# Performance work log

Measured on AMD Instinct MI355X. Metric: run time of the kernel, lower is better.

## Reference

```python
import jax, jax.numpy as jnp
import numpy as np

TOP_K = 2  # matches init kwarg top_k


def setup_inputs() -> dict:
    key = jax.random.key(0)
    k1, k2, k3, k4 = jax.random.split(key, 4)
    B, S, D, E = 4, 2048, 1024, 8
    x = jax.random.normal(k1, (B, S, D), dtype=jnp.float32)
    w_gate = jax.random.normal(k2, (D, E), dtype=jnp.float32) * 0.02
    w1 = jax.random.normal(k3, (E, D, 4 * D), dtype=jnp.float32) * 0.02
    w2 = jax.random.normal(k4, (E, 4 * D, D), dtype=jnp.float32) * 0.02
    return {"x": x, "w_gate": w_gate, "w1": w1, "w2": w2}


def reference(x, w_gate, w1, w2):
    # x: [B, S, D]; w_gate: [D, E]; w1: [E, D, 4D]; w2: [E, 4D, D]
    B, S, D = x.shape
    E = w1.shape[0]
    xt = x.reshape(-1, D)                      # [T, D], T = B*S
    T = xt.shape[0]

    logits = xt @ w_gate                       # [T, E]
    topk_vals, topk_idx = jax.lax.top_k(logits, TOP_K)  # [T, K]
    gates = jax.nn.softmax(topk_vals, axis=-1)          # [T, K]

    # Combine weights per (token, expert): scatter the top-k gates.
    comb = jnp.zeros((T, E), dtype=x.dtype)
    comb = comb.at[jnp.arange(T)[:, None], topk_idx].add(gates)  # [T, E]

    # Dense per-expert FFN over all tokens, masked by combine weight.
    # (Loop over the small fixed expert count; each iteration is a big GEMM.)
    out = jnp.zeros_like(xt)
    for e in range(E):
        h = jax.nn.relu(xt @ w1[e])            # [T, 4D]
        y = h @ w2[e]                          # [T, D]
        out = out + comb[:, e:e + 1] * y
    return out.reshape(B, S, D)
```

## Files before the change

kernel.cpp:

```cpp
#include <hip/hip_runtime.h>
#include <hip/hip_bf16.h>


#define T_TOK   8192
#define DIM     1024
#define NEXP    8
#define HID     4096
#define NASSIGN (T_TOK * 2)

typedef unsigned short ushort_t;
typedef __attribute__((ext_vector_type(8))) short bfrag;
typedef __attribute__((ext_vector_type(4))) float f32x4;

__device__ __forceinline__ ushort_t f2bf(float f) {
    union { float f; unsigned int u; } v; v.f = f;
    unsigned int r = v.u + 0x7FFFu + ((v.u >> 16) & 1u);
    return (ushort_t)(r >> 16);
}

__device__ __forceinline__ void async_load16(const void* g, void* l) {
    __builtin_amdgcn_global_load_lds(
        (const __attribute__((address_space(1))) unsigned int*)g,
        (__attribute__((address_space(3))) unsigned int*)l, 16, 0, 0);
}

__global__ __launch_bounds__(256)
void route_kern(const float* __restrict__ x, const float* __restrict__ wg,
                ushort_t* __restrict__ x_bf, int* __restrict__ topk,
                float* __restrict__ gates, int* __restrict__ counts)
{
    const int w = threadIdx.x >> 6, lane = threadIdx.x & 63;
    const int t = blockIdx.x * 4 + w;
    const float* xr = x + (size_t)t * DIM;
    float acc[8];
#pragma unroll
    for (int e = 0; e < 8; ++e) acc[e] = 0.f;

#pragma unroll
    for (int it = 0; it < 4; ++it) {
        const int j = it * 256 + lane * 4;
        float4 xv = *(const float4*)(xr + j);
        ushort4 xb;
        xb.x = f2bf(xv.x); xb.y = f2bf(xv.y); xb.z = f2bf(xv.z); xb.w = f2bf(xv.w);
        *(ushort4*)(x_bf + (size_t)t * DIM + j) = xb;
        const float xs[4] = {xv.x, xv.y, xv.z, xv.w};
#pragma unroll
        for (int jj = 0; jj < 4; ++jj) {
            float4 g0 = *(const float4*)(wg + (size_t)(j + jj) * 8);
            float4 g1 = *(const float4*)(wg + (size_t)(j + jj) * 8 + 4);
            acc[0] += xs[jj] * g0.x; acc[1] += xs[jj] * g0.y;
            acc[2] += xs[jj] * g0.z; acc[3] += xs[jj] * g0.w;
            acc[4] += xs[jj] * g1.x; acc[5] += xs[jj] * g1.y;
            acc[6] += xs[jj] * g1.z; acc[7] += xs[jj] * g1.w;
        }
    }
#pragma unroll
    for (int d = 1; d < 64; d <<= 1)
#pragma unroll
        for (int e = 0; e < 8; ++e) acc[e] += __shfl_xor(acc[e], d);

    if (lane == 0) {
        int i0 = 0; float v0 = acc[0];
#pragma unroll
        for (int e = 1; e < 8; ++e) if (acc[e] > v0) { v0 = acc[e]; i0 = e; }
        int i1 = -1; float v1 = -1e30f;
#pragma unroll
        for (int e = 0; e < 8; ++e) if (e != i0 && acc[e] > v1) { v1 = acc[e]; i1 = e; }
        float ex = __expf(v1 - v0);
        float inv = 1.f / (1.f + ex);
        topk[t * 2] = i0; topk[t * 2 + 1] = i1;
        gates[t * 2] = inv; gates[t * 2 + 1] = ex * inv;
        atomicAdd(&counts[i0], 1);
        atomicAdd(&counts[i1], 1);
    }
}

__global__ void scan_kern(const int* __restrict__ counts, int* __restrict__ offs,
                          int* __restrict__ cursors)
{
    if (threadIdx.x == 0) {
        int o = 0;
        for (int e = 0; e < NEXP; ++e) { offs[e] = o; cursors[e] = o; o += counts[e]; }
        offs[NEXP] = o;
    }
}

__global__ __launch_bounds__(256)
void scatter_kern(const int* __restrict__ topk, const float* __restrict__ gates,
                  int* __restrict__ cursors, int* __restrict__ tok_c,
                  float* __restrict__ gate_c)
{
    const int t = blockIdx.x * 256 + threadIdx.x;
#pragma unroll
    for (int k = 0; k < 2; ++k) {
        int e = topk[t * 2 + k];
        int pos = atomicAdd(&cursors[e], 1);
        tok_c[pos] = t;
        gate_c[pos] = gates[t * 2 + k];
    }
}

__global__ __launch_bounds__(256)
void transp_kern(const float* __restrict__ in, ushort_t* __restrict__ out, int K, int N)
{
    __shared__ float tile[64][65];
    const int e = blockIdx.z;
    const size_t ibase = (size_t)e * K * N, obase = (size_t)e * N * K;
    const int k0 = blockIdx.y * 64, n0 = blockIdx.x * 64;
    const int tid = threadIdx.x;

    const int r = tid >> 4, c4 = (tid & 15) * 4;
#pragma unroll
    for (int p = 0; p < 4; ++p) {
        int kk = p * 16 + r;
        float4 v = *(const float4*)(in + ibase + (size_t)(k0 + kk) * N + n0 + c4);
        tile[kk][c4] = v.x; tile[kk][c4 + 1] = v.y; tile[kk][c4 + 2] = v.z; tile[kk][c4 + 3] = v.w;
    }
    __syncthreads();
    const int nr = tid >> 6, kc = tid & 63;
#pragma unroll
    for (int p = 0; p < 16; ++p) {
        int nn = p * 4 + nr;
        out[obase + (size_t)(n0 + nn) * K + k0 + kc] = f2bf(tile[kc][nn]);
    }
}

template <int STAGE>
__global__ __launch_bounds__(256)
void gemm_kern(const ushort_t* __restrict__ A, const ushort_t* __restrict__ Bt,
               ushort_t* __restrict__ Hout, float* __restrict__ Out,
               const int* __restrict__ eoff, const int* __restrict__ tok_c,
               const float* __restrict__ gate_c, int K, int N)
{
    __shared__ ushort_t ldsA[128 * 64];
    __shared__ ushort_t ldsB[128 * 64];

    const int e = blockIdx.z;
    const int base = eoff[e];
    const int cnt = eoff[e + 1] - base;
    const int m0 = blockIdx.y * 128;
    if (m0 >= cnt) return;
    const int n0 = blockIdx.x * 128;

    const int tid = threadIdx.x;
    const int w = tid >> 6, lane = tid & 63;
    const int lhi = lane >> 4, llo = lane & 15;

    const ushort_t* asrc[4];
    const ushort_t* bsrc[4];
    int ldsoff[4];
    const ushort_t* Bbase = Bt + (size_t)e * (size_t)N * (size_t)K;
#pragma unroll
    for (int i = 0; i < 4; ++i) {
        int ci = ((i * 4 + w) << 6) + lane;
        int r = ci >> 3;
        int cb = (ci & 7) << 4;
        int sb = cb ^ ((r & 7) << 4);
        int gr = m0 + r; if (gr >= cnt) gr = cnt - 1;
        size_t arow = (STAGE == 1) ? (size_t)tok_c[base + gr] * DIM
                                   : (size_t)(base + gr) * HID;
        asrc[i] = A + arow + (sb >> 1);
        bsrc[i] = Bbase + (size_t)(n0 + r) * K + (sb >> 1);
        ldsoff[i] = (i * 4 + w) << 10;
    }

    f32x4 acc[4][4];
#pragma unroll
    for (int m = 0; m < 4; ++m)
#pragma unroll
        for (int n = 0; n < 4; ++n) acc[m][n] = (f32x4)(0.f);

    const int wr = (w >> 1) << 6;
    const int wc = (w & 1) << 6;

    for (int k0 = 0; k0 < K; k0 += 64) {
#pragma unroll
        for (int i = 0; i < 4; ++i) {
            async_load16(asrc[i] + k0, (char*)ldsA + ldsoff[i]);
            async_load16(bsrc[i] + k0, (char*)ldsB + ldsoff[i]);
        }
        __syncthreads();
#pragma unroll
        for (int s = 0; s < 2; ++s) {
            bfrag a[4], b[4];
            const int kb = (s << 6) + (lhi << 4);
#pragma unroll
            for (int m = 0; m < 4; ++m) {
                int row = wr + (m << 4) + llo;
                a[m] = *(const bfrag*)((const char*)ldsA + row * 128 + (kb ^ ((row & 7) << 4)));
            }
#pragma unroll
            for (int n = 0; n < 4; ++n) {
                int row = wc + (n << 4) + llo;
                b[n] = *(const bfrag*)((const char*)ldsB + row * 128 + (kb ^ ((row & 7) << 4)));
            }
#pragma unroll
            for (int m = 0; m < 4; ++m)
#pragma unroll
                for (int n = 0; n < 4; ++n)
                    acc[m][n] = __builtin_amdgcn_mfma_f32_16x16x32_bf16(a[m], b[n], acc[m][n], 0, 0, 0);
        }
        __syncthreads();
    }

    if (STAGE == 1) {
#pragma unroll
        for (int m = 0; m < 4; ++m)
#pragma unroll
            for (int i = 0; i < 4; ++i) {
                int row = wr + (m << 4) + (lhi << 2) + i;
                int gr = m0 + row;
                if (gr >= cnt) continue;
                size_t rb = (size_t)(base + gr) * HID + n0 + wc;
#pragma unroll
                for (int n = 0; n < 4; ++n) {
                    float v = acc[m][n][i];
                    Hout[rb + (n << 4) + llo] = f2bf(v > 0.f ? v : 0.f);
                }
            }
    } else {
#pragma unroll
        for (int m = 0; m < 4; ++m)
#pragma unroll
            for (int i = 0; i < 4; ++i) {
                int row = wr + (m << 4) + (lhi << 2) + i;
                int gr = m0 + row;
                if (gr >= cnt) continue;
                int tok = tok_c[base + gr];
                float g = gate_c[base + gr];
                size_t rb = (size_t)tok * DIM + n0 + wc;
#pragma unroll
                for (int n = 0; n < 4; ++n)
                    atomicAdd(&Out[rb + (n << 4) + llo], g * acc[m][n][i]);
            }
    }
}

extern "C" void kernel_launch(void* const* d_in, const int* in_sizes, int n_in,
                              void* d_out, int out_size, void* d_ws, size_t ws_size,
                              hipStream_t stream)
{
    const float* x  = (const float*)d_in[0];
    const float* wg = (const float*)d_in[1];
    const float* w1 = (const float*)d_in[2];
    const float* w2 = (const float*)d_in[3];
    float* out = (float*)d_out;

    char* ws = (char*)d_ws;
    ushort_t* x_bf = (ushort_t*)(ws + 0);
    ushort_t* w1t  = (ushort_t*)(ws + 16777216);
    ushort_t* w2t  = (ushort_t*)(ws + 83886080);
    ushort_t* h    = (ushort_t*)(ws + 150994944);
    char* ctrl     = ws + 285212672;
    int*   topk    = (int*)(ctrl);
    float* gates   = (float*)(ctrl + 65536);
    int*   tok_c   = (int*)(ctrl + 131072);
    float* gate_c  = (float*)(ctrl + 196608);
    int*   counts  = (int*)(ctrl + 262144);
    int*   offs    = (int*)(ctrl + 262144 + 64);
    int*   cursors = (int*)(ctrl + 262144 + 128);

    hipMemsetAsync(counts, 0, NEXP * sizeof(int), stream);
    hipMemsetAsync(out, 0, (size_t)T_TOK * DIM * sizeof(float), stream);

    route_kern<<<T_TOK / 4, 256, 0, stream>>>(x, wg, x_bf, topk, gates, counts);
    transp_kern<<<dim3(HID / 64, DIM / 64, NEXP), 256, 0, stream>>>(w1, w1t, DIM, HID);
    transp_kern<<<dim3(DIM / 64, HID / 64, NEXP), 256, 0, stream>>>(w2, w2t, HID, DIM);
    scan_kern<<<1, 64, 0, stream>>>(counts, offs, cursors);
    scatter_kern<<<T_TOK / 256, 256, 0, stream>>>(topk, gates, cursors, tok_c, gate_c);

    gemm_kern<1><<<dim3(HID / 128, 64, NEXP), 256, 0, stream>>>(
        x_bf, w1t, h, nullptr, offs, tok_c, gate_c, DIM, HID);
    gemm_kern<2><<<dim3(DIM / 128, 64, NEXP), 256, 0, stream>>>(
        h, w2t, nullptr, out, offs, tok_c, gate_c, HID, DIM);
}
```

Before: 761.5 us.

## Use 256x256 double-buffered GEMM tiles with XCD-aware block remapping

```diff
diff --git a/kernel.cpp b/kernel.cpp
--- a/kernel.cpp
+++ b/kernel.cpp
@@ -6,7 +6,6 @@
 #define DIM     1024
 #define NEXP    8
 #define HID     4096
-#define NASSIGN (T_TOK * 2)
 
 typedef unsigned short ushort_t;
 typedef __attribute__((ext_vector_type(8))) short bfrag;
@@ -125,93 +124,113 @@
     }
 }
 
-template <int STAGE>
-__global__ __launch_bounds__(256)
-void gemm_kern(const ushort_t* __restrict__ A, const ushort_t* __restrict__ Bt,
-               ushort_t* __restrict__ Hout, float* __restrict__ Out,
-               const int* __restrict__ eoff, const int* __restrict__ tok_c,
-               const float* __restrict__ gate_c, int K, int N)
-{
-    __shared__ ushort_t ldsA[128 * 64];
-    __shared__ ushort_t ldsB[128 * 64];
-
-    const int e = blockIdx.z;
+template <int STAGE, int NT, int NBLK>
+__global__ __launch_bounds__(512, 1)
+void gemm256(const ushort_t* __restrict__ A, const ushort_t* __restrict__ Bt,
+             ushort_t* __restrict__ Hout, float* __restrict__ Out,
+             const int* __restrict__ eoff, const int* __restrict__ tok_c,
+             const float* __restrict__ gate_c)
+{
+    constexpr int K = NT * 64;
+    constexpr int N = NBLK * 256;
+    constexpr int MB = 32;
+    __shared__ ushort_t lds[2][2][256 * 64];
+
+    const int nb = NEXP * MB * NBLK;
+    const int orig = blockIdx.x;
+    const int lg = (orig & 7) * (nb >> 3) + (orig >> 3);
+    const int e = lg / (MB * NBLK);
+    const int rem = lg - e * (MB * NBLK);
+    const int mblk = rem / NBLK;
+    const int nblk = rem - mblk * NBLK;
+
     const int base = eoff[e];
     const int cnt = eoff[e + 1] - base;
-    const int m0 = blockIdx.y * 128;
+    const int m0 = mblk * 256;
     if (m0 >= cnt) return;
-    const int n0 = blockIdx.x * 128;
+    const int n0 = nblk * 256;
 
     const int tid = threadIdx.x;
     const int w = tid >> 6, lane = tid & 63;
     const int lhi = lane >> 4, llo = lane & 15;
-
+    const int wm = (w >> 2) << 7;
+    const int wn = (w & 3) << 6;
+
+    const ushort_t* Bbase = Bt + (size_t)e * (size_t)N * (size_t)K;
     const ushort_t* asrc[4];
     const ushort_t* bsrc[4];
-    int ldsoff[4];
-    const ushort_t* Bbase = Bt + (size_t)e * (size_t)N * (size_t)K;
+    int lbase[4];
 #pragma unroll
     for (int i = 0; i < 4; ++i) {
-        int ci = ((i * 4 + w) << 6) + lane;
+        int ci = i * 512 + tid;
         int r = ci >> 3;
-        int cb = (ci & 7) << 4;
-        int sb = cb ^ ((r & 7) << 4);
+        int sb = ((ci & 7) << 4) ^ ((r & 7) << 4);
         int gr = m0 + r; if (gr >= cnt) gr = cnt - 1;
-        size_t arow = (STAGE == 1) ? (size_t)tok_c[base + gr] * DIM
-                                   : (size_t)(base + gr) * HID;
+        size_t arow = (STAGE == 1) ? (size_t)tok_c[base + gr] * (size_t)K
+                                   : (size_t)(base + gr) * (size_t)K;
         asrc[i] = A + arow + (sb >> 1);
         bsrc[i] = Bbase + (size_t)(n0 + r) * K + (sb >> 1);
-        ldsoff[i] = (i * 4 + w) << 10;
-    }
-
-    f32x4 acc[4][4];
-#pragma unroll
-    for (int m = 0; m < 4; ++m)
+        lbase[i] = (i * 8 + w) << 10;
+    }
+
+    f32x4 acc[8][4];
+#pragma unroll
+    for (int m = 0; m < 8; ++m)
 #pragma unroll
         for (int n = 0; n < 4; ++n) acc[m][n] = (f32x4)(0.f);
 
-    const int wr = (w >> 1) << 6;
-    const int wc = (w & 1) << 6;
-
-    for (int k0 = 0; k0 < K; k0 += 64) {
-#pragma unroll
-        for (int i = 0; i < 4; ++i) {
-            async_load16(asrc[i] + k0, (char*)ldsA + ldsoff[i]);
-            async_load16(bsrc[i] + k0, (char*)ldsB + ldsoff[i]);
+#pragma unroll
+    for (int i = 0; i < 4; ++i) {
+        async_load16(asrc[i], (char*)lds[0][0] + lbase[i]);
+        async_load16(bsrc[i], (char*)lds[0][1] + lbase[i]);
+    }
+    __syncthreads();
+
+    int cur = 0;
+    for (int t = 0; t < NT; ++t) {
+        if (t + 1 < NT) {
+            const int k0 = (t + 1) << 6;
+#pragma unroll
+            for (int i = 0; i < 4; ++i) {
+                async_load16(asrc[i] + k0, (char*)lds[cur ^ 1][0] + lbase[i]);
+                async_load16(bsrc[i] + k0, (char*)lds[cur ^ 1][1] + lbase[i]);
+            }
         }
-        __syncthreads();
-#pragma unroll
-        for (int s = 0; s < 2; ++s) {
-            bfrag a[4], b[4];
-            const int kb = (s << 6) + (lhi << 4);
-#pragma unroll
-            for (int m = 0; m < 4; ++m) {
-                int row = wr + (m << 4) + llo;
-                a[m] = *(const bfrag*)((const char*)ldsA + row * 128 + (kb ^ ((row & 7) << 4)));
+        const char* pA = (const char*)lds[cur][0];
+        const char* pB = (const char*)lds[cur][1];
+#pragma unroll
+        for (int ks = 0; ks < 2; ++ks) {
+            const int kb = (ks << 6) + (lhi << 4);
+            bfrag a[8], b[4];
+#pragma unroll
+            for (int m = 0; m < 8; ++m) {
+                int row = wm + (m << 4) + llo;
+                a[m] = *(const bfrag*)(pA + row * 128 + (kb ^ ((row & 7) << 4)));
             }
 #pragma unroll
             for (int n = 0; n < 4; ++n) {
-                int row = wc + (n << 4) + llo;
-                b[n] = *(const bfrag*)((const char*)ldsB + row * 128 + (kb ^ ((row & 7) << 4)));
-            }
-#pragma unroll
-            for (int m = 0; m < 4; ++m)
+                int row = wn + (n << 4) + llo;
+                b[n] = *(const bfrag*)(pB + row * 128 + (kb ^ ((row & 7) << 4)));
+            }
+#pragma unroll
+            for (int m = 0; m < 8; ++m)
 #pragma unroll
                 for (int n = 0; n < 4; ++n)
                     acc[m][n] = __builtin_amdgcn_mfma_f32_16x16x32_bf16(a[m], b[n], acc[m][n], 0, 0, 0);
         }
         __syncthreads();
+        cur ^= 1;
     }
 
     if (STAGE == 1) {
 #pragma unroll
-        for (int m = 0; m < 4; ++m)
+        for (int m = 0; m < 8; ++m)
 #pragma unroll
             for (int i = 0; i < 4; ++i) {
-                int row = wr + (m << 4) + (lhi << 2) + i;
+                int row = wm + (m << 4) + (lhi << 2) + i;
                 int gr = m0 + row;
                 if (gr >= cnt) continue;
-                size_t rb = (size_t)(base + gr) * HID + n0 + wc;
+                size_t rb = (size_t)(base + gr) * (size_t)N + n0 + wn;
 #pragma unroll
                 for (int n = 0; n < 4; ++n) {
                     float v = acc[m][n][i];
@@ -220,15 +239,15 @@
             }
     } else {
 #pragma unroll
-        for (int m = 0; m < 4; ++m)
+        for (int m = 0; m < 8; ++m)
 #pragma unroll
             for (int i = 0; i < 4; ++i) {
-                int row = wr + (m << 4) + (lhi << 2) + i;
+                int row = wm + (m << 4) + (lhi << 2) + i;
                 int gr = m0 + row;
                 if (gr >= cnt) continue;
                 int tok = tok_c[base + gr];
                 float g = gate_c[base + gr];
-                size_t rb = (size_t)tok * DIM + n0 + wc;
+                size_t rb = (size_t)tok * (size_t)N + n0 + wn;
 #pragma unroll
                 for (int n = 0; n < 4; ++n)
                     atomicAdd(&Out[rb + (n << 4) + llo], g * acc[m][n][i]);
@@ -269,8 +288,8 @@
     scan_kern<<<1, 64, 0, stream>>>(counts, offs, cursors);
     scatter_kern<<<T_TOK / 256, 256, 0, stream>>>(topk, gates, cursors, tok_c, gate_c);
 
-    gemm_kern<1><<<dim3(HID / 128, 64, NEXP), 256, 0, stream>>>(
-        x_bf, w1t, h, nullptr, offs, tok_c, gate_c, DIM, HID);
-    gemm_kern<2><<<dim3(DIM / 128, 64, NEXP), 256, 0, stream>>>(
-        h, w2t, nullptr, out, offs, tok_c, gate_c, HID, DIM);
-}
+    gemm256<1, 16, 16><<<NEXP * 32 * 16, 512, 0, stream>>>(
+        x_bf, w1t, h, nullptr, offs, tok_c, gate_c);
+    gemm256<2, 64, 4><<<NEXP * 32 * 4, 512, 0, stream>>>(
+        h, w2t, nullptr, out, offs, tok_c, gate_c);
+}
```

After: 765.3 us. Within noise of the previous version (+0.5%).

## Add split-K for down-projection, XCD-aware block remap, and vectorized transpose stores

Applied to the files above, without the earlier changes.

```diff
diff --git a/kernel.cpp b/kernel.cpp
--- a/kernel.cpp
+++ b/kernel.cpp
@@ -6,7 +6,6 @@
 #define DIM     1024
 #define NEXP    8
 #define HID     4096
-#define NASSIGN (T_TOK * 2)
 
 typedef unsigned short ushort_t;
 typedef __attribute__((ext_vector_type(8))) short bfrag;
@@ -117,30 +116,44 @@
         tile[kk][c4] = v.x; tile[kk][c4 + 1] = v.y; tile[kk][c4 + 2] = v.z; tile[kk][c4 + 3] = v.w;
     }
     __syncthreads();
-    const int nr = tid >> 6, kc = tid & 63;
-#pragma unroll
-    for (int p = 0; p < 16; ++p) {
-        int nn = p * 4 + nr;
-        out[obase + (size_t)(n0 + nn) * K + k0 + kc] = f2bf(tile[kc][nn]);
-    }
-}
-
-template <int STAGE>
+    const int k8 = (tid & 7) * 8, nr = tid >> 3;
+#pragma unroll
+    for (int p = 0; p < 2; ++p) {
+        int nn = p * 32 + nr;
+        bfrag v;
+#pragma unroll
+        for (int j = 0; j < 8; ++j) v[j] = (short)f2bf(tile[k8 + j][nn]);
+        *(bfrag*)(out + obase + (size_t)(n0 + nn) * K + k0 + k8) = v;
+    }
+}
+
+template <int STAGE, int NTK, int NBF, int SPLITK, int KF, int NF>
 __global__ __launch_bounds__(256)
 void gemm_kern(const ushort_t* __restrict__ A, const ushort_t* __restrict__ Bt,
                ushort_t* __restrict__ Hout, float* __restrict__ Out,
                const int* __restrict__ eoff, const int* __restrict__ tok_c,
-               const float* __restrict__ gate_c, int K, int N)
-{
+               const float* __restrict__ gate_c)
+{
+    constexpr int MBF = 64;
     __shared__ ushort_t ldsA[128 * 64];
     __shared__ ushort_t ldsB[128 * 64];
 
-    const int e = blockIdx.z;
+    constexpr int nb = NEXP * MBF * NBF;
+    const int orig = blockIdx.x;
+    const int lg = (orig & 7) * (nb >> 3) + (orig >> 3);
+    const int e = lg / (MBF * NBF);
+    const int rem = lg - e * (MBF * NBF);
+    const int mblk = rem / NBF;
+    const int nidx = rem - mblk * NBF;
+    const int nblk = nidx / SPLITK;
+    const int ks = nidx - nblk * SPLITK;
+    const int kbeg = ks * NTK * 64;
+
     const int base = eoff[e];
     const int cnt = eoff[e + 1] - base;
-    const int m0 = blockIdx.y * 128;
+    const int m0 = mblk * 128;
     if (m0 >= cnt) return;
-    const int n0 = blockIdx.x * 128;
+    const int n0 = nblk * 128;
 
     const int tid = threadIdx.x;
     const int w = tid >> 6, lane = tid & 63;
@@ -149,7 +162,7 @@
     const ushort_t* asrc[4];
     const ushort_t* bsrc[4];
     int ldsoff[4];
-    const ushort_t* Bbase = Bt + (size_t)e * (size_t)N * (size_t)K;
+    const ushort_t* Bbase = Bt + (size_t)e * (size_t)NF * (size_t)KF;
 #pragma unroll
     for (int i = 0; i < 4; ++i) {
         int ci = ((i * 4 + w) << 6) + lane;
@@ -157,10 +170,10 @@
         int cb = (ci & 7) << 4;
         int sb = cb ^ ((r & 7) << 4);
         int gr = m0 + r; if (gr >= cnt) gr = cnt - 1;
-        size_t arow = (STAGE == 1) ? (size_t)tok_c[base + gr] * DIM
-                                   : (size_t)(base + gr) * HID;
+        size_t arow = (STAGE == 1) ? (size_t)tok_c[base + gr] * (size_t)KF
+                                   : (size_t)(base + gr) * (size_t)KF;
         asrc[i] = A + arow + (sb >> 1);
-        bsrc[i] = Bbase + (size_t)(n0 + r) * K + (sb >> 1);
+        bsrc[i] = Bbase + (size_t)(n0 + r) * KF + (sb >> 1);
         ldsoff[i] = (i * 4 + w) << 10;
     }
 
@@ -173,7 +186,8 @@
     const int wr = (w >> 1) << 6;
     const int wc = (w & 1) << 6;
 
-    for (int k0 = 0; k0 < K; k0 += 64) {
+    for (int kt = 0; kt < NTK; ++kt) {
+        const int k0 = kbeg + kt * 64;
 #pragma unroll
         for (int i = 0; i < 4; ++i) {
             async_load16(asrc[i] + k0, (char*)ldsA + ldsoff[i]);
@@ -211,7 +225,7 @@
                 int row = wr + (m << 4) + (lhi << 2) + i;
                 int gr = m0 + row;
                 if (gr >= cnt) continue;
-                size_t rb = (size_t)(base + gr) * HID + n0 + wc;
+                size_t rb = (size_t)(base + gr) * (size_t)NF + n0 + wc;
 #pragma unroll
                 for (int n = 0; n < 4; ++n) {
                     float v = acc[m][n][i];
@@ -228,7 +242,7 @@
                 if (gr >= cnt) continue;
                 int tok = tok_c[base + gr];
                 float g = gate_c[base + gr];
-                size_t rb = (size_t)tok * DIM + n0 + wc;
+                size_t rb = (size_t)tok * (size_t)NF + n0 + wc;
 #pragma unroll
                 for (int n = 0; n < 4; ++n)
                     atomicAdd(&Out[rb + (n << 4) + llo], g * acc[m][n][i]);
@@ -269,8 +283,8 @@
     scan_kern<<<1, 64, 0, stream>>>(counts, offs, cursors);
     scatter_kern<<<T_TOK / 256, 256, 0, stream>>>(topk, gates, cursors, tok_c, gate_c);
 
-    gemm_kern<1><<<dim3(HID / 128, 64, NEXP), 256, 0, stream>>>(
-        x_bf, w1t, h, nullptr, offs, tok_c, gate_c, DIM, HID);
-    gemm_kern<2><<<dim3(DIM / 128, 64, NEXP), 256, 0, stream>>>(
-        h, w2t, nullptr, out, offs, tok_c, gate_c, HID, DIM);
-}
+    gemm_kern<1, 16, 32, 1, 1024, 4096><<<NEXP * 64 * 32, 256, 0, stream>>>(
+        x_bf, w1t, h, nullptr, offs, tok_c, gate_c);
+    gemm_kern<2, 32, 16, 2, 4096, 1024><<<NEXP * 64 * 16, 256, 0, stream>>>(
+        h, w2t, nullptr, out, offs, tok_c, gate_c);
+}
```

Result: slower. 883.0 us (+15.9%).
